# Kernel tuning notes

Hardware: AMD Instinct MI355X
Metric: run time of the kernel (lower is better)

The kernel has to match this reference:

```python
import jax, jax.numpy as jnp
import numpy as np

B, G, M, N, RBF, H = 8, 1024, 8, 2048, 50, 128
CUT_LO, CUT_HI = 0.0, 5.0
F = RBF * M * M  # 3200 = in_features of the basis projections


def setup_inputs() -> dict:
    key = jax.random.key(0)
    ks = jax.random.split(key, 8)
    x = jax.random.normal(ks[0], (B, N, 3), dtype=jnp.float32)
    # mapping: linear mixing of fine particles into G groups of M coarse particles
    W_map = jax.random.normal(ks[1], (G, M, N), dtype=jnp.float32) / np.float32(np.sqrt(N))
    W_left = jax.random.normal(ks[2], (H, F), dtype=jnp.float32) / np.float32(np.sqrt(F))
    W_right = jax.random.normal(ks[3], (H, F), dtype=jnp.float32) / np.float32(np.sqrt(F))
    fc1_w = jax.random.normal(ks[4], (H, H), dtype=jnp.float32) / np.float32(np.sqrt(H))
    fc1_b = jax.random.normal(ks[5], (H,), dtype=jnp.float32) * 0.01
    fc2_w = jax.random.normal(ks[6], (1, H), dtype=jnp.float32) / np.float32(np.sqrt(H))
    fc2_b = jax.random.normal(ks[7], (1,), dtype=jnp.float32) * 0.01
    return {"x": x, "W_map": W_map, "W_left": W_left, "W_right": W_right,
            "fc1_w": fc1_w, "fc1_b": fc1_b, "fc2_w": fc2_w, "fc2_b": fc2_b}


def reference(x, W_map, W_left, W_right, fc1_w, fc1_b, fc2_w, fc2_b):
    # ExpNormalSmearing constants (torchmd-net defaults, non-trainable)
    alpha = np.float32(5.0 / (CUT_HI - CUT_LO))
    means = jnp.linspace(np.float32(np.exp(-CUT_HI + CUT_LO)), 1.0, RBF, dtype=jnp.float32)
    beta = np.float32((2.0 / RBF * (1.0 - np.exp(-CUT_HI + CUT_LO))) ** -2)

    # mapping: [B,N,3] -> coarse grained [B,G,M,3]
    xc = jnp.einsum('gmn,bnd->bgmd', W_map, x)
    # pairwise deltas within each group: [B,G,M,M,3]
    delta = xc[:, :, None, :, :] - xc[:, :, :, None, :]
    dn = jnp.sqrt(jnp.sum(delta ** 2, axis=-1, keepdims=True) + 1e-5)  # [B,G,M,M,1]
    # cosine cutoff * exp-normal RBF -> [B,G,M,M,RBF]
    cutoff = 0.5 * (jnp.cos(dn * jnp.pi / CUT_HI) + 1.0) * (dn < CUT_HI)
    sm = cutoff * jnp.exp(-beta * (jnp.exp(alpha * (CUT_LO - dn)) - means) ** 2)
    sm = sm / (dn + 1e-5) ** 2
    # outer-product basis: [B,G,M,M,RBF,3] -> [B,G,F,3]
    basis = (delta[..., None, :] * sm[..., None]).reshape(B, G, F, 3)
    # dual projections over the F axis (Linear applied on swapped axes)
    left = jnp.einsum('hf,bgfd->bghd', W_left, basis)   # [B,G,H,3]
    right = jnp.einsum('hf,bgfd->bghd', W_right, basis)  # [B,G,H,3]
    att = jnp.sum(left * right, axis=-1) + 1e-5          # [B,G,H]
    att = jax.nn.logsumexp(att, axis=-2)                  # pool over groups -> [B,H]
    h = jax.nn.silu(att @ fc1_w.T + fc1_b)
    return h @ fc2_w.T + fc2_b  # [B,1]
```

## Files before the change

kernel.cpp:

```cpp
#include <hip/hip_runtime.h>
#include <hip/hip_bf16.h>
#include <math.h>

#define B_   8
#define G_   1024
#define M_   8
#define N_   2048
#define RBF_ 50
#define H_   128
#define PP_  28
#define RPP  64
#define KTOT (PP_*RPP)
#define KSTEPS (KTOT/32)
#define TPB  32

#define OFF_A    0
#define SZ_A     (KSTEPS*16*64*8/2)
#define OFF_XC   (OFF_A + SZ_A)
#define SZ_XC    (B_*G_*M_*3)
#define OFF_ATT  (OFF_XC + SZ_XC)
#define SZ_ATT   (B_*H_*G_)
#define OFF_PART (OFF_ATT + SZ_ATT)
#define SZ_PART  (B_*8*H_*2)

#define M0_   0.006737946999085467f
#define STEP_ 0.020270858224508f
#define BETA_ 633.5087862829640f
#define C2_   25.68448448181152f
#define C3_   0.26031300425529f
#define BC_   0.59416621404589f

typedef __attribute__((ext_vector_type(8))) short s8v;
typedef __attribute__((ext_vector_type(4))) float f4v;

__device__ const int c_pi[28] = {0,0,0,0,0,0,0,1,1,1,1,1,1,2,2,2,2,2,3,3,3,3,4,4,4,5,5,6};
__device__ const int c_pj[28] = {1,2,3,4,5,6,7,2,3,4,5,6,7,3,4,5,6,7,4,5,6,7,5,6,7,6,7,7};

__device__ __forceinline__ unsigned short f2bf(float f) {
    unsigned int b = __float_as_uint(f);
    return (unsigned short)((b + 0x7FFFu + ((b >> 16) & 1u)) >> 16);
}

__global__ __launch_bounds__(256) void k_folda(const float* __restrict__ Wl,
                                               const float* __restrict__ Wr,
                                               float* __restrict__ ws) {
    int t = blockIdx.x * 256 + threadIdx.x;
    int lane = t & 63;
    int mt = (t >> 6) & 15;
    int kstep = t >> 10;
    int pp = kstep >> 1;
    int row = mt * 16 + (lane & 15);
    int side = row >> 7, h = row & 127;
    int r0 = (kstep & 1) * 32 + (lane >> 4) * 8;
    int i = c_pi[pp], j = c_pj[pp];
    const float* src = side ? Wr : Wl;
    const float* pij = src + h * 3200 + (i * 8 + j) * 50;
    const float* pji = src + h * 3200 + (j * 8 + i) * 50;
    s8v v;
#pragma unroll
    for (int e = 0; e < 8; ++e) {
        int r = r0 + e;
        float f = (r < 50) ? (pij[r] - pji[r]) : 0.f;
        v[e] = (short)f2bf(f);
    }
    ((s8v*)(ws + OFF_A))[t] = v;
}

__global__ __launch_bounds__(256) void k_xc(const float* __restrict__ x,
                                            const float* __restrict__ Wm,
                                            float* __restrict__ ws) {
    float* xc = ws + OFF_XC;
    int rg = blockIdx.x >> 4;
    int ns = blockIdx.x & 15;
    int row = rg * 256 + threadIdx.x;
    int n0 = ns * 128;
    float acc[24];
#pragma unroll
    for (int c = 0; c < 24; ++c) acc[c] = 0.f;
    const float* wrow = Wm + (size_t)row * 2048 + n0;
    for (int k = 0; k < 32; ++k) {
        float4 w4 = *(const float4*)(wrow + k * 4);
#pragma unroll
        for (int j = 0; j < 4; ++j) {
            float wk = (j == 0) ? w4.x : (j == 1) ? w4.y : (j == 2) ? w4.z : w4.w;
            const float* xp = x + (size_t)(n0 + k*4 + j) * 3;
#pragma unroll
            for (int bb = 0; bb < 8; ++bb) {
                acc[bb*3+0] += wk * xp[bb*6144 + 0];
                acc[bb*3+1] += wk * xp[bb*6144 + 1];
                acc[bb*3+2] += wk * xp[bb*6144 + 2];
            }
        }
    }
#pragma unroll
    for (int bb = 0; bb < 8; ++bb)
#pragma unroll
        for (int d = 0; d < 3; ++d)
            atomicAdd(&xc[(size_t)bb*24576 + row*3 + d], acc[bb*3+d]);
}

__global__ __launch_bounds__(256, 1) void k_main(float* __restrict__ ws) {
    __shared__ __align__(16) char smem[128 * 97 * 4];
    s8v*   Bf = (s8v*)smem;
    float* P  = (float*)smem;

    const float* xc = ws + OFF_XC;
    const s8v* A8 = (const s8v*)(ws + OFF_A);
    float* att = ws + OFF_ATT;

    int tid = threadIdx.x;
    int wave = tid >> 6, lane = tid & 63;
    int p0 = blockIdx.x * TPB;

    int pairL = tid >> 3;
    int sub = tid & 7;
    int rblk = sub >> 1;
    int dh = sub & 1;
    int pairG = p0 + pairL;
    int bb = pairG >> 10, gg = pairG & 1023;
    const float* xp = xc + ((size_t)bb * 8192 + gg * 8) * 3;

    int mtile[4] = {2*wave, 2*wave+1, 2*wave+8, 2*wave+9};

    f4v acc[4][6];
#pragma unroll
    for (int mi = 0; mi < 4; ++mi)
#pragma unroll
        for (int nt = 0; nt < 6; ++nt) acc[mi][nt] = (f4v)0.f;

    for (int pp = 0; pp < 28; ++pp) {
        s8v afr[2][4];
#pragma unroll
        for (int ksl = 0; ksl < 2; ++ksl)
#pragma unroll
            for (int mi = 0; mi < 4; ++mi)
                afr[ksl][mi] = A8[((pp*2 + ksl)*16 + mtile[mi])*64 + lane];

        int i = c_pi[pp], j = c_pj[pp];
        float dx = xp[j*3+0] - xp[i*3+0];
        float dy = xp[j*3+1] - xp[i*3+1];
        float dz = xp[j*3+2] - xp[i*3+2];
        float dn = sqrtf(dx*dx + dy*dy + dz*dz + 1e-5f);
        float pref = 0.f;
        if (dn < 5.0f) pref = 0.5f * (cosf(dn * 0.62831853071795865f) + 1.0f);
        float dinv = dn + 1e-5f;
        pref /= (dinv * dinv);
        float ex = expf(-dn);
        int r0 = rblk * 16;
        float d0 = ex - (M0_ + (float)r0 * STEP_);
        float sm    = pref * expf(-BETA_ * d0 * d0);
        float ratio = expf(C2_ * d0 - C3_);
        float smv[16];
#pragma unroll
        for (int q = 0; q < 16; ++q) { smv[q] = sm; sm *= ratio; ratio *= BC_; }

        float dd[2];
        int ndw;
        if (dh == 0) { dd[0] = dx; dd[1] = dy; ndw = 2; }
        else         { dd[0] = dz; dd[1] = 0.f; ndw = 1; }
#pragma unroll
        for (int w = 0; w < 2; ++w) {
            if (w >= ndw) break;
            int d = (dh == 0) ? w : 2;
            int col = pairL * 3 + d;
            int nt = col >> 4, cl = col & 15;
#pragma unroll
            for (int half = 0; half < 2; ++half) {
                int rb = r0 + half * 8;
                int ks = rb >> 5;
                int lf = (((rb >> 3) & 3) << 4) | cl;
                s8v v;
#pragma unroll
                for (int e = 0; e < 8; ++e)
                    v[e] = (short)f2bf(smv[half*8 + e] * dd[w]);
                Bf[(ks*6 + nt)*64 + lf] = v;
            }
        }
        __syncthreads();

#pragma unroll
        for (int ksl = 0; ksl < 2; ++ksl)
#pragma unroll
            for (int nt = 0; nt < 6; ++nt) {
                s8v bfr = Bf[(ksl*6 + nt)*64 + lane];
#pragma unroll
                for (int mi = 0; mi < 4; ++mi)
                    acc[mi][nt] = __builtin_amdgcn_mfma_f32_16x16x32_bf16(
                        afr[ksl][mi], bfr, acc[mi][nt], 0, 0, 0);
            }
        __syncthreads();
    }

#pragma unroll
    for (int mi = 0; mi < 2; ++mi)
#pragma unroll
        for (int nt = 0; nt < 6; ++nt)
#pragma unroll
            for (int reg = 0; reg < 4; ++reg) {
                int row = mtile[mi]*16 + (lane >> 4)*4 + reg;
                int col = nt*16 + (lane & 15);
                P[row*97 + col] = acc[mi][nt][reg];
            }
    __syncthreads();
#pragma unroll
    for (int mi = 2; mi < 4; ++mi)
#pragma unroll
        for (int nt = 0; nt < 6; ++nt)
#pragma unroll
            for (int reg = 0; reg < 4; ++reg) {
                int row = (mtile[mi] - 8)*16 + (lane >> 4)*4 + reg;
                int col = nt*16 + (lane & 15);
                P[row*97 + col] *= acc[mi][nt][reg];
            }
    __syncthreads();
    int h = tid & 127;
    int pr0 = (tid >> 7) * 16;
#pragma unroll
    for (int q = 0; q < 16; ++q) {
        int pr = pr0 + q;
        float a = P[h*97 + pr*3] + P[h*97 + pr*3 + 1] + P[h*97 + pr*3 + 2] + 1e-5f;
        att[(size_t)(p0 + pr) * 128 + h] = a;
    }
}

__global__ __launch_bounds__(256) void k_lse(float* __restrict__ ws) {
    const float* att = ws + OFF_ATT;
    float* part = ws + OFF_PART;
    int blk = blockIdx.x;
    int b = blk >> 3, gblk = blk & 7;
    int tid = threadIdx.x;
    int h = tid & 127, gh = tid >> 7;
    const float* p = att + ((size_t)(b*1024 + gblk*128 + gh*64))*128 + h;
    float m = -1e30f, s = 0.f;
    for (int q = 0; q < 64; ++q) {
        float v = p[(size_t)q * 128];
        float nm = fmaxf(m, v);
        s = s * expf(m - nm) + expf(v - nm);
        m = nm;
    }
    __shared__ float mm[256], ss[256];
    mm[tid] = m; ss[tid] = s;
    __syncthreads();
    if (gh == 0) {
        float m2 = mm[tid + 128], s2 = ss[tid + 128];
        float Mv = fmaxf(m, m2);
        float Sv = s * expf(m - Mv) + s2 * expf(m2 - Mv);
        *(float2*)&part[((size_t)(b*8 + gblk)*128 + h)*2] = make_float2(Mv, Sv);
    }
}

__global__ __launch_bounds__(128) void k_mlp(const float* __restrict__ ws,
                                             const float* __restrict__ f1w,
                                             const float* __restrict__ f1b,
                                             const float* __restrict__ f2w,
                                             const float* __restrict__ f2b,
                                             float* __restrict__ out) {
    const float* part = ws + OFF_PART;
    int b = blockIdx.x, h = threadIdx.x;
    float ms[8], sv[8], Mv = -1e30f;
#pragma unroll
    for (int k = 0; k < 8; ++k) {
        float2 v = *(const float2*)&part[((size_t)(b*8 + k)*128 + h)*2];
        ms[k] = v.x; sv[k] = v.y;
        Mv = fmaxf(Mv, v.x);
    }
    float Sv = 0.f;
#pragma unroll
    for (int k = 0; k < 8; ++k) Sv += sv[k] * expf(ms[k] - Mv);
    float lse = Mv + logf(Sv);
    __shared__ float ls[128];
    ls[h] = lse;
    __syncthreads();
    float acc = f1b[h];
    for (int k = 0; k < 128; ++k) acc += f1w[h*128 + k] * ls[k];
    float v = acc / (1.f + expf(-acc));
    __shared__ float red[128];
    red[h] = v * f2w[h];
    __syncthreads();
    for (int st = 64; st > 0; st >>= 1) {
        if (h < st) red[h] += red[h + st];
        __syncthreads();
    }
    if (h == 0) out[b] = red[0] + f2b[0];
}

extern "C" void kernel_launch(void* const* d_in, const int* in_sizes, int n_in,
                              void* d_out, int out_size, void* d_ws, size_t ws_size,
                              hipStream_t stream) {
    const float* x   = (const float*)d_in[0];
    const float* Wm  = (const float*)d_in[1];
    const float* Wl  = (const float*)d_in[2];
    const float* Wr  = (const float*)d_in[3];
    const float* f1w = (const float*)d_in[4];
    const float* f1b = (const float*)d_in[5];
    const float* f2w = (const float*)d_in[6];
    const float* f2b = (const float*)d_in[7];
    float* ws  = (float*)d_ws;
    float* out = (float*)d_out;

    hipMemsetAsync(ws + OFF_XC, 0, SZ_XC * sizeof(float), stream);

    k_folda<<<224, 256, 0, stream>>>(Wl, Wr, ws);
    k_xc   <<<512, 256, 0, stream>>>(x, Wm, ws);
    k_main <<<256, 256, 0, stream>>>(ws);
    k_lse  <<<64,  256, 0, stream>>>(ws);
    k_mlp  <<<8,   128, 0, stream>>>(ws, f1w, f1b, f2w, f2b, out);
}
```

Before: 224.8 us.

## Rewrite coarse-graining kernel without atomics, double waves in main kernel, widen LSE split

The mapping kernel is rewritten so each block owns 16 full rows of W_map. It stages x in LDS with register prefetch, reduces within a wave through shared memory, and stores directly, removing the memset and the atomicAdds. The main MFMA kernel now runs 512 threads per block: each wave handles one row tile pair, and each thread computes one spatial component, which lowers per-thread register and ALU load. The group logsumexp is split across more blocks (256 instead of 64), and a lighter barrier macro replaces __syncthreads.

```diff
diff --git a/kernel.cpp b/kernel.cpp
--- a/kernel.cpp
+++ b/kernel.cpp
@@ -10,8 +10,7 @@
 #define H_   128
 #define PP_  28
 #define RPP  64
-#define KTOT (PP_*RPP)
-#define KSTEPS (KTOT/32)
+#define KSTEPS (PP_*RPP/32)
 #define TPB  32
 
 #define OFF_A    0
@@ -21,7 +20,7 @@
 #define OFF_ATT  (OFF_XC + SZ_XC)
 #define SZ_ATT   (B_*H_*G_)
 #define OFF_PART (OFF_ATT + SZ_ATT)
-#define SZ_PART  (B_*8*H_*2)
+#define SZ_PART  (B_*32*H_*2)
 
 #define M0_   0.006737946999085467f
 #define STEP_ 0.020270858224508f
@@ -32,6 +31,11 @@
 
 typedef __attribute__((ext_vector_type(8))) short s8v;
 typedef __attribute__((ext_vector_type(4))) float f4v;
+
+#define LBAR() do { \
+    asm volatile("s_waitcnt lgkmcnt(0)\n\ts_barrier" ::: "memory"); \
+    __builtin_amdgcn_sched_barrier(0); \
+} while (0)
 
 __device__ const int c_pi[28] = {0,0,0,0,0,0,0,1,1,1,1,1,1,2,2,2,2,2,3,3,3,3,4,4,4,5,5,6};
 __device__ const int c_pj[28] = {1,2,3,4,5,6,7,2,3,4,5,6,7,3,4,5,6,7,4,5,6,7,5,6,7,6,7,7};
@@ -66,40 +70,105 @@
     ((s8v*)(ws + OFF_A))[t] = v;
 }
 
-__global__ __launch_bounds__(256) void k_xc(const float* __restrict__ x,
-                                            const float* __restrict__ Wm,
-                                            float* __restrict__ ws) {
+__global__ __launch_bounds__(256, 2) void k_xc(const float* __restrict__ x,
+                                               const float* __restrict__ Wm,
+                                               float* __restrict__ ws) {
+    __shared__ float4 x_s[6][256];
+    __shared__ float  red[4][24][68];
     float* xc = ws + OFF_XC;
-    int rg = blockIdx.x >> 4;
-    int ns = blockIdx.x & 15;
-    int row = rg * 256 + threadIdx.x;
-    int n0 = ns * 128;
-    float acc[24];
-#pragma unroll
-    for (int c = 0; c < 24; ++c) acc[c] = 0.f;
-    const float* wrow = Wm + (size_t)row * 2048 + n0;
-    for (int k = 0; k < 32; ++k) {
-        float4 w4 = *(const float4*)(wrow + k * 4);
-#pragma unroll
-        for (int j = 0; j < 4; ++j) {
-            float wk = (j == 0) ? w4.x : (j == 1) ? w4.y : (j == 2) ? w4.z : w4.w;
-            const float* xp = x + (size_t)(n0 + k*4 + j) * 3;
-#pragma unroll
-            for (int bb = 0; bb < 8; ++bb) {
-                acc[bb*3+0] += wk * xp[bb*6144 + 0];
-                acc[bb*3+1] += wk * xp[bb*6144 + 1];
-                acc[bb*3+2] += wk * xp[bb*6144 + 2];
-            }
-        }
-    }
-#pragma unroll
-    for (int bb = 0; bb < 8; ++bb)
-#pragma unroll
-        for (int d = 0; d < 3; ++d)
-            atomicAdd(&xc[(size_t)bb*24576 + row*3 + d], acc[bb*3+d]);
-}
-
-__global__ __launch_bounds__(256, 1) void k_main(float* __restrict__ ws) {
+
+    int tid = threadIdx.x;
+    int wave = tid >> 6, lane = tid & 63;
+    int rowbase = blockIdx.x * 16 + wave * 4;
+
+    f4v acc[4][6];
+#pragma unroll
+    for (int r = 0; r < 4; ++r)
+#pragma unroll
+        for (int p = 0; p < 6; ++p) acc[r][p] = (f4v)0.f;
+
+#pragma unroll
+    for (int p = 0; p < 6; ++p) {
+        int bd0 = p * 4;
+        float4 v;
+        v.x = x[(bd0/3)*6144     + tid*3 + (bd0%3)];
+        v.y = x[((bd0+1)/3)*6144 + tid*3 + ((bd0+1)%3)];
+        v.z = x[((bd0+2)/3)*6144 + tid*3 + ((bd0+2)%3)];
+        v.w = x[((bd0+3)/3)*6144 + tid*3 + ((bd0+3)%3)];
+        x_s[p][tid] = v;
+    }
+    LBAR();
+
+#pragma unroll 1
+    for (int nc = 0; nc < 8; ++nc) {
+        int n0 = nc * 256;
+        float4 pf[6];
+        if (nc < 7) {
+            int n1 = n0 + 256;
+#pragma unroll
+            for (int p = 0; p < 6; ++p) {
+                int bd0 = p * 4;
+                pf[p].x = x[(bd0/3)*6144     + (n1+tid)*3 + (bd0%3)];
+                pf[p].y = x[((bd0+1)/3)*6144 + (n1+tid)*3 + ((bd0+1)%3)];
+                pf[p].z = x[((bd0+2)/3)*6144 + (n1+tid)*3 + ((bd0+2)%3)];
+                pf[p].w = x[((bd0+3)/3)*6144 + (n1+tid)*3 + ((bd0+3)%3)];
+            }
+        }
+        float wv[4][4];
+#pragma unroll
+        for (int r = 0; r < 4; ++r) {
+            const float* wrow = Wm + (size_t)(rowbase + r) * 2048 + n0 + lane;
+#pragma unroll
+            for (int k = 0; k < 4; ++k) wv[r][k] = wrow[k * 64];
+        }
+#pragma unroll
+        for (int k = 0; k < 4; ++k) {
+            int nn = k * 64 + lane;
+#pragma unroll
+            for (int p = 0; p < 6; ++p) {
+                float4 xq = x_s[p][nn];
+#pragma unroll
+                for (int r = 0; r < 4; ++r) {
+                    acc[r][p].x += wv[r][k] * xq.x;
+                    acc[r][p].y += wv[r][k] * xq.y;
+                    acc[r][p].z += wv[r][k] * xq.z;
+                    acc[r][p].w += wv[r][k] * xq.w;
+                }
+            }
+        }
+        LBAR();
+        if (nc < 7) {
+#pragma unroll
+            for (int p = 0; p < 6; ++p) x_s[p][tid] = pf[p];
+        }
+        LBAR();
+    }
+
+    int cc = lane;
+#pragma unroll 1
+    for (int r = 0; r < 4; ++r) {
+#pragma unroll
+        for (int p = 0; p < 6; ++p) {
+            red[wave][p*4+0][lane] = acc[r][p].x;
+            red[wave][p*4+1][lane] = acc[r][p].y;
+            red[wave][p*4+2][lane] = acc[r][p].z;
+            red[wave][p*4+3][lane] = acc[r][p].w;
+        }
+        if (cc < 24) {
+            float s = 0.f;
+#pragma unroll
+            for (int k = 0; k < 16; ++k) {
+                float4 v = *(const float4*)&red[wave][cc][k*4];
+                s += (v.x + v.y) + (v.z + v.w);
+            }
+            int row = rowbase + r;
+            int b = cc / 3, d = cc - b * 3;
+            xc[(size_t)b*24576 + row*3 + d] = s;
+        }
+    }
+}
+
+__global__ __launch_bounds__(512, 1) void k_main(float* __restrict__ ws) {
     __shared__ __align__(16) char smem[128 * 97 * 4];
     s8v*   Bf = (s8v*)smem;
     float* P  = (float*)smem;
@@ -112,57 +181,49 @@
     int wave = tid >> 6, lane = tid & 63;
     int p0 = blockIdx.x * TPB;
 
-    int pairL = tid >> 3;
-    int sub = tid & 7;
-    int rblk = sub >> 1;
-    int dh = sub & 1;
+    int pairL = tid >> 4;
+    int sub = tid & 15;
+    int rblk = sub >> 2;
+    int dsel = sub & 3;
     int pairG = p0 + pairL;
     int bb = pairG >> 10, gg = pairG & 1023;
     const float* xp = xc + ((size_t)bb * 8192 + gg * 8) * 3;
 
-    int mtile[4] = {2*wave, 2*wave+1, 2*wave+8, 2*wave+9};
-
-    f4v acc[4][6];
-#pragma unroll
-    for (int mi = 0; mi < 4; ++mi)
+    f4v acc[2][6];
+#pragma unroll
+    for (int mi = 0; mi < 2; ++mi)
 #pragma unroll
         for (int nt = 0; nt < 6; ++nt) acc[mi][nt] = (f4v)0.f;
 
+#pragma unroll 1
     for (int pp = 0; pp < 28; ++pp) {
-        s8v afr[2][4];
-#pragma unroll
-        for (int ksl = 0; ksl < 2; ++ksl)
-#pragma unroll
-            for (int mi = 0; mi < 4; ++mi)
-                afr[ksl][mi] = A8[((pp*2 + ksl)*16 + mtile[mi])*64 + lane];
-
-        int i = c_pi[pp], j = c_pj[pp];
-        float dx = xp[j*3+0] - xp[i*3+0];
-        float dy = xp[j*3+1] - xp[i*3+1];
-        float dz = xp[j*3+2] - xp[i*3+2];
-        float dn = sqrtf(dx*dx + dy*dy + dz*dz + 1e-5f);
-        float pref = 0.f;
-        if (dn < 5.0f) pref = 0.5f * (cosf(dn * 0.62831853071795865f) + 1.0f);
-        float dinv = dn + 1e-5f;
-        pref /= (dinv * dinv);
-        float ex = expf(-dn);
-        int r0 = rblk * 16;
-        float d0 = ex - (M0_ + (float)r0 * STEP_);
-        float sm    = pref * expf(-BETA_ * d0 * d0);
-        float ratio = expf(C2_ * d0 - C3_);
-        float smv[16];
-#pragma unroll
-        for (int q = 0; q < 16; ++q) { smv[q] = sm; sm *= ratio; ratio *= BC_; }
-
-        float dd[2];
-        int ndw;
-        if (dh == 0) { dd[0] = dx; dd[1] = dy; ndw = 2; }
-        else         { dd[0] = dz; dd[1] = 0.f; ndw = 1; }
-#pragma unroll
-        for (int w = 0; w < 2; ++w) {
-            if (w >= ndw) break;
-            int d = (dh == 0) ? w : 2;
-            int col = pairL * 3 + d;
+        s8v afr[2][2];
+#pragma unroll
+        for (int ksl = 0; ksl < 2; ++ksl) {
+            afr[ksl][0] = A8[((pp*2 + ksl)*16 + wave    )*64 + lane];
+            afr[ksl][1] = A8[((pp*2 + ksl)*16 + wave + 8)*64 + lane];
+        }
+
+        if (dsel < 3) {
+            int i = c_pi[pp], j = c_pj[pp];
+            float dx = xp[j*3+0] - xp[i*3+0];
+            float dy = xp[j*3+1] - xp[i*3+1];
+            float dz = xp[j*3+2] - xp[i*3+2];
+            float dn = sqrtf(dx*dx + dy*dy + dz*dz + 1e-5f);
+            float pref = 0.f;
+            if (dn < 5.0f) pref = 0.5f * (cosf(dn * 0.62831853071795865f) + 1.0f);
+            float dinv = dn + 1e-5f;
+            pref /= (dinv * dinv);
+            float ex = expf(-dn);
+            int r0 = rblk * 16;
+            float d0 = ex - (M0_ + (float)r0 * STEP_);
+            float sm    = pref * expf(-BETA_ * d0 * d0);
+            float ratio = expf(C2_ * d0 - C3_);
+            float smv[16];
+#pragma unroll
+            for (int q = 0; q < 16; ++q) { smv[q] = sm; sm *= ratio; ratio *= BC_; }
+            float dd = (dsel == 0) ? dx : (dsel == 1) ? dy : dz;
+            int col = pairL * 3 + dsel;
             int nt = col >> 4, cl = col & 15;
 #pragma unroll
             for (int half = 0; half < 2; ++half) {
@@ -172,11 +233,11 @@
                 s8v v;
 #pragma unroll
                 for (int e = 0; e < 8; ++e)
-                    v[e] = (short)f2bf(smv[half*8 + e] * dd[w]);
+                    v[e] = (short)f2bf(smv[half*8 + e] * dd);
                 Bf[(ks*6 + nt)*64 + lf] = v;
             }
         }
-        __syncthreads();
+        LBAR();
 
 #pragma unroll
         for (int ksl = 0; ksl < 2; ++ksl)
@@ -184,39 +245,34 @@
             for (int nt = 0; nt < 6; ++nt) {
                 s8v bfr = Bf[(ksl*6 + nt)*64 + lane];
 #pragma unroll
-                for (int mi = 0; mi < 4; ++mi)
+                for (int mi = 0; mi < 2; ++mi)
                     acc[mi][nt] = __builtin_amdgcn_mfma_f32_16x16x32_bf16(
                         afr[ksl][mi], bfr, acc[mi][nt], 0, 0, 0);
             }
-        __syncthreads();
-    }
-
-#pragma unroll
-    for (int mi = 0; mi < 2; ++mi)
-#pragma unroll
-        for (int nt = 0; nt < 6; ++nt)
-#pragma unroll
-            for (int reg = 0; reg < 4; ++reg) {
-                int row = mtile[mi]*16 + (lane >> 4)*4 + reg;
-                int col = nt*16 + (lane & 15);
-                P[row*97 + col] = acc[mi][nt][reg];
-            }
-    __syncthreads();
-#pragma unroll
-    for (int mi = 2; mi < 4; ++mi)
-#pragma unroll
-        for (int nt = 0; nt < 6; ++nt)
-#pragma unroll
-            for (int reg = 0; reg < 4; ++reg) {
-                int row = (mtile[mi] - 8)*16 + (lane >> 4)*4 + reg;
-                int col = nt*16 + (lane & 15);
-                P[row*97 + col] *= acc[mi][nt][reg];
-            }
+        LBAR();
+    }
+
+#pragma unroll
+    for (int nt = 0; nt < 6; ++nt)
+#pragma unroll
+        for (int reg = 0; reg < 4; ++reg) {
+            int row = wave*16 + (lane >> 4)*4 + reg;
+            int col = nt*16 + (lane & 15);
+            P[row*97 + col] = acc[0][nt][reg];
+        }
+#pragma unroll
+    for (int nt = 0; nt < 6; ++nt)
+#pragma unroll
+        for (int reg = 0; reg < 4; ++reg) {
+            int row = wave*16 + (lane >> 4)*4 + reg;
+            int col = nt*16 + (lane & 15);
+            P[row*97 + col] *= acc[1][nt][reg];
+        }
     __syncthreads();
     int h = tid & 127;
-    int pr0 = (tid >> 7) * 16;
-#pragma unroll
-    for (int q = 0; q < 16; ++q) {
+    int pr0 = (tid >> 7) * 8;
+#pragma unroll
+    for (int q = 0; q < 8; ++q) {
         int pr = pr0 + q;
         float a = P[h*97 + pr*3] + P[h*97 + pr*3 + 1] + P[h*97 + pr*3 + 2] + 1e-5f;
         att[(size_t)(p0 + pr) * 128 + h] = a;
@@ -227,12 +283,13 @@
     const float* att = ws + OFF_ATT;
     float* part = ws + OFF_PART;
     int blk = blockIdx.x;
-    int b = blk >> 3, gblk = blk & 7;
+    int b = blk >> 5, gblk = blk & 31;
     int tid = threadIdx.x;
     int h = tid & 127, gh = tid >> 7;
-    const float* p = att + ((size_t)(b*1024 + gblk*128 + gh*64))*128 + h;
+    const float* p = att + ((size_t)(b*1024 + gblk*32 + gh*16))*128 + h;
     float m = -1e30f, s = 0.f;
-    for (int q = 0; q < 64; ++q) {
+#pragma unroll
+    for (int q = 0; q < 16; ++q) {
         float v = p[(size_t)q * 128];
         float nm = fmaxf(m, v);
         s = s * expf(m - nm) + expf(v - nm);
@@ -245,7 +302,7 @@
         float m2 = mm[tid + 128], s2 = ss[tid + 128];
         float Mv = fmaxf(m, m2);
         float Sv = s * expf(m - Mv) + s2 * expf(m2 - Mv);
-        *(float2*)&part[((size_t)(b*8 + gblk)*128 + h)*2] = make_float2(Mv, Sv);
+        *(float2*)&part[((size_t)(b*32 + gblk)*128 + h)*2] = make_float2(Mv, Sv);
     }
 }
 
@@ -257,16 +314,14 @@
                                              float* __restrict__ out) {
     const float* part = ws + OFF_PART;
     int b = blockIdx.x, h = threadIdx.x;
-    float ms[8], sv[8], Mv = -1e30f;
-#pragma unroll
-    for (int k = 0; k < 8; ++k) {
-        float2 v = *(const float2*)&part[((size_t)(b*8 + k)*128 + h)*2];
-        ms[k] = v.x; sv[k] = v.y;
-        Mv = fmaxf(Mv, v.x);
-    }
-    float Sv = 0.f;
-#pragma unroll
-    for (int k = 0; k < 8; ++k) Sv += sv[k] * expf(ms[k] - Mv);
+    float Mv = -1e30f, Sv = 0.f;
+#pragma unroll
+    for (int k = 0; k < 32; ++k) {
+        float2 v = *(const float2*)&part[((size_t)(b*32 + k)*128 + h)*2];
+        float nm = fmaxf(Mv, v.x);
+        Sv = Sv * expf(Mv - nm) + v.y * expf(v.x - nm);
+        Mv = nm;
+    }
     float lse = Mv + logf(Sv);
     __shared__ float ls[128];
     ls[h] = lse;
@@ -298,11 +353,9 @@
     float* ws  = (float*)d_ws;
     float* out = (float*)d_out;
 
-    hipMemsetAsync(ws + OFF_XC, 0, SZ_XC * sizeof(float), stream);
-
     k_folda<<<224, 256, 0, stream>>>(Wl, Wr, ws);
     k_xc   <<<512, 256, 0, stream>>>(x, Wm, ws);
-    k_main <<<256, 256, 0, stream>>>(ws);
-    k_lse  <<<64,  256, 0, stream>>>(ws);
+    k_main <<<256, 512, 0, stream>>>(ws);
+    k_lse  <<<256, 256, 0, stream>>>(ws);
     k_mlp  <<<8,   128, 0, stream>>>(ws, f1w, f1b, f2w, f2b, out);
 }
```

After: 224.1 us. About the same (-0.3%).
